# Performance work log

Measured on AMD Instinct MI355X. Metric: run time of the kernel, lower is better.

## Reference

```python
import jax, jax.numpy as jnp
import numpy as np

B, D, T, K = 32768, 1024, 100, 4  # batch, input_dim, num_trees, 2**(tree_depth-1)

def setup_inputs() -> dict:
    key = jax.random.key(0)
    k1, k2, k3, k4, k5 = jax.random.split(key, 5)
    s1 = 1.0 / np.sqrt(D)
    s2 = 1.0 / np.sqrt(K)
    return {
        "x": jax.random.normal(k1, (B, D), dtype=jnp.float32),
        "W1": jax.random.uniform(k2, (T, K, D), jnp.float32, -s1, s1),  # per-tree first Linear
        "b1": jax.random.uniform(k3, (T, K), jnp.float32, -s1, s1),
        "final_weight": jnp.full((T,), 1.0 / T, dtype=jnp.float32),
        "fc_w": jax.random.uniform(k4, (2, K), jnp.float32, -s2, s2),
        "fc_b": jax.random.uniform(k5, (2,), jnp.float32, -s2, s2),
    }

def reference(x, W1, b1, final_weight, fc_w, fc_b):
    # split_probs for all trees at once: [B, T, K]
    split = jnp.einsum("bd,tkd->btk", x, W1) + b1[None, :, :]
    leaf = jax.nn.sigmoid(split)  # tree[1] is Sigmoid applied to split_probs
    # sum(split.unsqueeze(1)*leaf.unsqueeze(2), -1) == leaf * sum_k(split)
    tree_out = leaf * jnp.sum(split, axis=-1, keepdims=True)  # [B, T, K]
    weighted = jnp.einsum("btk,t->bk", tree_out, final_weight)  # [B, K]
    logits = weighted @ fc_w.T + fc_b  # [B, 2]
    return logits
```

## Files before the change

kernel.cpp:

```cpp
#include <hip/hip_runtime.h>
#include <hip/hip_bf16.h>


typedef __bf16 bf16x8 __attribute__((ext_vector_type(8)));
typedef float f32x4 __attribute__((ext_vector_type(4)));

#define B_ROWS 32768
#define D_DIM  1024
#define N_COLS 400
#define BM     128
#define BK     64
#define NCHUNK 16
#define THREADS 640
#define NTPW 5
#define MT   4

__device__ __forceinline__ unsigned short f2bf(float f) {
    unsigned int u = __float_as_uint(f);
    u += 0x7FFFu + ((u >> 16) & 1u);
    return (unsigned short)(u >> 16);
}
__device__ __forceinline__ unsigned int pk2(float a, float b) {
    return (unsigned int)f2bf(a) | ((unsigned int)f2bf(b) << 16);
}
__device__ __forceinline__ uint4 cvt8u(float4 a, float4 b) {
    uint4 u;
    u.x = pk2(a.x, a.y); u.y = pk2(a.z, a.w);
    u.z = pk2(b.x, b.y); u.w = pk2(b.z, b.w);
    return u;
}
__device__ __forceinline__ bf16x8 cvt8(float4 a, float4 b) {
    return __builtin_bit_cast(bf16x8, cvt8u(a, b));
}

__global__ void cvt_f32_bf16_kernel(const float* __restrict__ in,
                                    unsigned short* __restrict__ out) {
    size_t i = ((size_t)blockIdx.x * 256 + threadIdx.x) * 8;
    float4 v0 = *reinterpret_cast<const float4*>(in + i);
    float4 v1 = *reinterpret_cast<const float4*>(in + i + 4);
    *reinterpret_cast<uint4*>(out + i) = cvt8u(v0, v1);
}

__device__ __forceinline__ void gl_lds16(const unsigned short* g,
                                         unsigned short* l) {
    __builtin_amdgcn_global_load_lds(
        (const __attribute__((address_space(1))) unsigned int*)g,
        (__attribute__((address_space(3))) unsigned int*)l,
        16, 0, 0);
}

#define FOR_N_(OP, m) OP(m,0) OP(m,1) OP(m,2) OP(m,3) OP(m,4)
#define FOR_MN(OP) FOR_N_(OP,0) FOR_N_(OP,1) FOR_N_(OP,2) FOR_N_(OP,3)

#define DECL_ACC(m,n) f32x4 acc##m##n = {};
#define MFMA_MN(m,n) acc##m##n = __builtin_amdgcn_mfma_f32_16x16x32_bf16( \
        afr##m, bfr##n, acc##m##n, 0, 0, 0);

template <int MODE>
__global__ __launch_bounds__(THREADS, 1) void xgb_v8(
    const float* __restrict__ x,
    const void*  __restrict__ b_any,
    const float* __restrict__ b1,
    const float* __restrict__ fw,
    const float* __restrict__ fcw,
    const float* __restrict__ fcb,
    float* __restrict__ out)
{
    __shared__ __align__(16) unsigned short Abuf[2][BM * BK];
    __shared__ __align__(16) unsigned short Bbuf[2][N_COLS * BK];
    __shared__ float Pbuf[BM * NTPW * 2];

    const int tid  = threadIdx.x;
    const int wave = tid >> 6;
    const int lane = tid & 63;
    const int quad = lane >> 4;
    const int l15  = lane & 15;
    const int mh   = wave / 5;
    const int nf   = wave % 5;
    const int row0 = blockIdx.x * BM;

    FOR_MN(DECL_ACC)

    if (MODE == 0) {
        const unsigned short* w1b = (const unsigned short*)b_any;

#define BDECL(t) const unsigned short* bsrc##t; int bdst##t; \
        { const int s_ = wave + 10 * (t); const int rr_ = lane >> 3; \
          const int cc_ = ((lane & 7) - rr_) & 7; \
          bsrc##t = w1b + (size_t)(s_ * 8 + rr_) * D_DIM + cc_ * 8; \
          bdst##t = s_ * 512; }
        BDECL(0) BDECL(1) BDECL(2) BDECL(3) BDECL(4)

        const int r0a = tid >> 3,          c0a = tid & 7;
        const int r1a = (tid + 640) >> 3,  c1a = (tid + 640) & 7;
        const bool hasU1 = (tid < 384);
        const float* asrc0 = x + (size_t)(row0 + r0a) * D_DIM + c0a * 8;
        const float* asrc1 = x + (size_t)(row0 + r1a) * D_DIM + c1a * 8;
        const int adst0 = r0a * 64 + ((c0a + r0a) & 7) * 8;
        const int adst1 = r1a * 64 + ((c1a + r1a) & 7) * 8;
        float4 areg00, areg01, areg10, areg11;

#define LOADA(kc) do { \
        areg00 = *reinterpret_cast<const float4*>(asrc0 + (kc));     \
        areg01 = *reinterpret_cast<const float4*>(asrc0 + (kc) + 4); \
        if (hasU1) { \
            areg10 = *reinterpret_cast<const float4*>(asrc1 + (kc));     \
            areg11 = *reinterpret_cast<const float4*>(asrc1 + (kc) + 4); \
        } } while (0)

#define WRITEA(Ab) do { \
        *reinterpret_cast<uint4*>((Ab) + adst0) = cvt8u(areg00, areg01); \
        if (hasU1) \
            *reinterpret_cast<uint4*>((Ab) + adst1) = cvt8u(areg10, areg11); \
        } while (0)

#define STAGEB(kc, Bb) do { \
        gl_lds16(bsrc0 + (kc), (Bb) + bdst0); \
        gl_lds16(bsrc1 + (kc), (Bb) + bdst1); \
        gl_lds16(bsrc2 + (kc), (Bb) + bdst2); \
        gl_lds16(bsrc3 + (kc), (Bb) + bdst3); \
        gl_lds16(bsrc4 + (kc), (Bb) + bdst4); } while (0)

#define LOAD_AFR(m) { const int row_ = mh * 64 + (m) * 16 + l15; \
        const int p_ = (quad + h * 4 + row_) & 7; \
        afr##m = *reinterpret_cast<const bf16x8*>(Ab_ + row_ * 64 + p_ * 8); }
#define LOAD_BFR(n) { const int row_ = (nf * NTPW + (n)) * 16 + l15; \
        const int p_ = (quad + h * 4 + row_) & 7; \
        bfr##n = *reinterpret_cast<const bf16x8*>(Bb_ + row_ * 64 + p_ * 8); }

        LOADA(0);
        STAGEB(0, Bbuf[0]);
        WRITEA(Abuf[0]);

        #pragma unroll 1
        for (int c = 0; c < NCHUNK; ++c) {
            const int cur = c & 1;
            const unsigned short* Ab_ = Abuf[cur];
            const unsigned short* Bb_ = Bbuf[cur];
            __syncthreads();
            if (c + 1 < NCHUNK) {
                LOADA((c + 1) * BK);
                STAGEB((c + 1) * BK, Bbuf[1 - cur]);
            }
            #pragma unroll
            for (int h = 0; h < 2; ++h) {
                bf16x8 afr0, afr1, afr2, afr3;
                bf16x8 bfr0, bfr1, bfr2, bfr3, bfr4;
                LOAD_AFR(0) LOAD_AFR(1) LOAD_AFR(2) LOAD_AFR(3)
                LOAD_BFR(0) LOAD_BFR(1) LOAD_BFR(2) LOAD_BFR(3) LOAD_BFR(4)
                FOR_MN(MFMA_MN)
            }
            if (c + 1 < NCHUNK) WRITEA(Abuf[1 - cur]);
        }
    } else {
        const float* af = x + (size_t)(row0 + mh * 64 + l15) * D_DIM + quad * 8;
        const float* bf32 = (const float*)b_any
                          + (size_t)((nf * NTPW) * 16 + l15) * D_DIM + quad * 8;
        for (int step = 0; step < 32; ++step) {
            const int off = step * 32;
            bf16x8 afr0, afr1, afr2, afr3;
            bf16x8 bfr0, bfr1, bfr2, bfr3, bfr4;
#define LOAD_AFR2(m) { \
            float4 a0_ = *reinterpret_cast<const float4*>(af + (size_t)(m) * 16 * D_DIM + off); \
            float4 a1_ = *reinterpret_cast<const float4*>(af + (size_t)(m) * 16 * D_DIM + off + 4); \
            afr##m = cvt8(a0_, a1_); }
#define LOAD_BFR2(n) { \
            float4 b0_ = *reinterpret_cast<const float4*>(bf32 + (size_t)(n) * 16 * D_DIM + off); \
            float4 b1_ = *reinterpret_cast<const float4*>(bf32 + (size_t)(n) * 16 * D_DIM + off + 4); \
            bfr##n = cvt8(b0_, b1_); }
            LOAD_AFR2(0) LOAD_AFR2(1) LOAD_AFR2(2) LOAD_AFR2(3)
            LOAD_BFR2(0) LOAD_BFR2(1) LOAD_BFR2(2) LOAD_BFR2(3) LOAD_BFR2(4)
            FOR_MN(MFMA_MN)
        }
    }

    const float fcw0 = fcw[l15 & 3];
    const float fcw1 = fcw[4 + (l15 & 3)];

#define PRE_N(n) \
    const float bias##n = b1[(nf * NTPW + (n)) * 16 + l15]; \
    const float tw##n   = fw[((nf * NTPW + (n)) * 16 + l15) >> 2];
    PRE_N(0) PRE_N(1) PRE_N(2) PRE_N(3) PRE_N(4)

#define EPI_TERM(m,r,n) { \
        const float split_ = acc##m##n[r] + bias##n; \
        float s_ = split_; \
        s_ += __shfl_xor(s_, 1); \
        s_ += __shfl_xor(s_, 2); \
        const float leaf_ = 1.0f / (1.0f + __expf(-split_)); \
        const float val_ = tw##n * leaf_ * s_; \
        q0 += val_ * fcw0; q1 += val_ * fcw1; }

#define EPI_ONE(m,r) { \
        float q0 = 0.f, q1 = 0.f; \
        EPI_TERM(m,r,0) EPI_TERM(m,r,1) EPI_TERM(m,r,2) \
        EPI_TERM(m,r,3) EPI_TERM(m,r,4) \
        q0 += __shfl_xor(q0, 1); q0 += __shfl_xor(q0, 2); \
        q0 += __shfl_xor(q0, 4); q0 += __shfl_xor(q0, 8); \
        q1 += __shfl_xor(q1, 1); q1 += __shfl_xor(q1, 2); \
        q1 += __shfl_xor(q1, 4); q1 += __shfl_xor(q1, 8); \
        const int row_ = mh * 64 + (m) * 16 + quad * 4 + (r); \
        if (l15 == 0) Pbuf[(row_ * NTPW + nf) * 2 + 0] = q0; \
        if (l15 == 1) Pbuf[(row_ * NTPW + nf) * 2 + 1] = q1; }

#define EPI_M(m) EPI_ONE(m,0) EPI_ONE(m,1) EPI_ONE(m,2) EPI_ONE(m,3)
    EPI_M(0) EPI_M(1) EPI_M(2) EPI_M(3)

    __syncthreads();

    if (tid < 2 * BM) {
        const int r = tid >> 1, j = tid & 1;
        float s = fcb[j];
        #pragma unroll
        for (int w = 0; w < NTPW; ++w)
            s += Pbuf[(r * NTPW + w) * 2 + j];
        out[(row0 + r) * 2 + j] = s;
    }
}

extern "C" void kernel_launch(void* const* d_in, const int* in_sizes, int n_in,
                              void* d_out, int out_size, void* d_ws, size_t ws_size,
                              hipStream_t stream) {
    const float* x   = (const float*)d_in[0];
    const float* W1  = (const float*)d_in[1];
    const float* b1  = (const float*)d_in[2];
    const float* fw  = (const float*)d_in[3];
    const float* fcw = (const float*)d_in[4];
    const float* fcb = (const float*)d_in[5];
    float* out = (float*)d_out;

    const size_t w1_elems = (size_t)N_COLS * D_DIM;
    if (ws_size >= w1_elems * sizeof(unsigned short)) {
        unsigned short* w1b = (unsigned short*)d_ws;
        cvt_f32_bf16_kernel<<<(int)(w1_elems / 2048), 256, 0, stream>>>(W1, w1b);
        xgb_v8<0><<<B_ROWS / BM, THREADS, 0, stream>>>(
            x, (const void*)w1b, b1, fw, fcw, fcb, out);
    } else {
        xgb_v8<2><<<B_ROWS / BM, THREADS, 0, stream>>>(
            x, (const void*)W1, b1, fw, fcw, fcb, out);
    }
}
```

Baseline: 235.5 us.

## Shrink block to 64 rows and 32-wide K chunks for multi-block occupancy

Halves the row tile and K chunk, cuts the block to five waves that each own one N-fragment group, and raises launch bounds to three blocks per CU. LDS swizzling is reworked for 32-wide rows. The goal is more resident blocks so they can hide global-load and sync latency. The cost is twice as many K iterations and barriers, and each W1 tile is now reused across fewer rows, so W1 traffic rises.

```diff
diff --git a/kernel.cpp b/kernel.cpp
--- a/kernel.cpp
+++ b/kernel.cpp
@@ -8,10 +8,10 @@
 #define B_ROWS 32768
 #define D_DIM  1024
 #define N_COLS 400
-#define BM     128
-#define BK     64
-#define NCHUNK 16
-#define THREADS 640
+#define BM     64
+#define BK     32
+#define NCHUNK 32
+#define THREADS 320
 #define NTPW 5
 #define MT   4
 
@@ -57,7 +57,7 @@
         afr##m, bfr##n, acc##m##n, 0, 0, 0);
 
 template <int MODE>
-__global__ __launch_bounds__(THREADS, 1) void xgb_v8(
+__global__ __launch_bounds__(THREADS, 3) void xgb_v9(
     const float* __restrict__ x,
     const void*  __restrict__ b_any,
     const float* __restrict__ b1,
@@ -75,8 +75,7 @@
     const int lane = tid & 63;
     const int quad = lane >> 4;
     const int l15  = lane & 15;
-    const int mh   = wave / 5;
-    const int nf   = wave % 5;
+    const int nf   = wave;
     const int row0 = blockIdx.x * BM;
 
     FOR_MN(DECL_ACC)
@@ -85,33 +84,25 @@
         const unsigned short* w1b = (const unsigned short*)b_any;
 
 #define BDECL(t) const unsigned short* bsrc##t; int bdst##t; \
-        { const int s_ = wave + 10 * (t); const int rr_ = lane >> 3; \
-          const int cc_ = ((lane & 7) - rr_) & 7; \
-          bsrc##t = w1b + (size_t)(s_ * 8 + rr_) * D_DIM + cc_ * 8; \
+        { const int s_ = wave + 5 * (t); const int rb_ = s_ * 16 + (lane >> 2); \
+          const int cc_ = ((lane & 3) - (rb_ >> 1)) & 3; \
+          bsrc##t = w1b + (size_t)rb_ * D_DIM + cc_ * 8; \
           bdst##t = s_ * 512; }
         BDECL(0) BDECL(1) BDECL(2) BDECL(3) BDECL(4)
 
-        const int r0a = tid >> 3,          c0a = tid & 7;
-        const int r1a = (tid + 640) >> 3,  c1a = (tid + 640) & 7;
-        const bool hasU1 = (tid < 384);
+        const int r0a = tid >> 2, c0a = tid & 3;
+        const bool doA = (tid < 256);
         const float* asrc0 = x + (size_t)(row0 + r0a) * D_DIM + c0a * 8;
-        const float* asrc1 = x + (size_t)(row0 + r1a) * D_DIM + c1a * 8;
-        const int adst0 = r0a * 64 + ((c0a + r0a) & 7) * 8;
-        const int adst1 = r1a * 64 + ((c1a + r1a) & 7) * 8;
-        float4 areg00, areg01, areg10, areg11;
-
-#define LOADA(kc) do { \
+        const int adst0 = r0a * 32 + ((c0a + (r0a >> 1)) & 3) * 8;
+        float4 areg00, areg01;
+
+#define LOADA(kc) do { if (doA) { \
         areg00 = *reinterpret_cast<const float4*>(asrc0 + (kc));     \
         areg01 = *reinterpret_cast<const float4*>(asrc0 + (kc) + 4); \
-        if (hasU1) { \
-            areg10 = *reinterpret_cast<const float4*>(asrc1 + (kc));     \
-            areg11 = *reinterpret_cast<const float4*>(asrc1 + (kc) + 4); \
         } } while (0)
 
-#define WRITEA(Ab) do { \
+#define WRITEA(Ab) do { if (doA) \
         *reinterpret_cast<uint4*>((Ab) + adst0) = cvt8u(areg00, areg01); \
-        if (hasU1) \
-            *reinterpret_cast<uint4*>((Ab) + adst1) = cvt8u(areg10, areg11); \
         } while (0)
 
 #define STAGEB(kc, Bb) do { \
@@ -121,12 +112,12 @@
         gl_lds16(bsrc3 + (kc), (Bb) + bdst3); \
         gl_lds16(bsrc4 + (kc), (Bb) + bdst4); } while (0)
 
-#define LOAD_AFR(m) { const int row_ = mh * 64 + (m) * 16 + l15; \
-        const int p_ = (quad + h * 4 + row_) & 7; \
-        afr##m = *reinterpret_cast<const bf16x8*>(Ab_ + row_ * 64 + p_ * 8); }
+#define LOAD_AFR(m) { const int row_ = (m) * 16 + l15; \
+        const int p_ = (quad + (row_ >> 1)) & 3; \
+        afr##m = *reinterpret_cast<const bf16x8*>(Ab_ + row_ * 32 + p_ * 8); }
 #define LOAD_BFR(n) { const int row_ = (nf * NTPW + (n)) * 16 + l15; \
-        const int p_ = (quad + h * 4 + row_) & 7; \
-        bfr##n = *reinterpret_cast<const bf16x8*>(Bb_ + row_ * 64 + p_ * 8); }
+        const int p_ = (quad + (row_ >> 1)) & 3; \
+        bfr##n = *reinterpret_cast<const bf16x8*>(Bb_ + row_ * 32 + p_ * 8); }
 
         LOADA(0);
         STAGEB(0, Bbuf[0]);
@@ -142,8 +133,7 @@
                 LOADA((c + 1) * BK);
                 STAGEB((c + 1) * BK, Bbuf[1 - cur]);
             }
-            #pragma unroll
-            for (int h = 0; h < 2; ++h) {
+            {
                 bf16x8 afr0, afr1, afr2, afr3;
                 bf16x8 bfr0, bfr1, bfr2, bfr3, bfr4;
                 LOAD_AFR(0) LOAD_AFR(1) LOAD_AFR(2) LOAD_AFR(3)
@@ -153,7 +143,7 @@
             if (c + 1 < NCHUNK) WRITEA(Abuf[1 - cur]);
         }
     } else {
-        const float* af = x + (size_t)(row0 + mh * 64 + l15) * D_DIM + quad * 8;
+        const float* af = x + (size_t)(row0 + l15) * D_DIM + quad * 8;
         const float* bf32 = (const float*)b_any
                           + (size_t)((nf * NTPW) * 16 + l15) * D_DIM + quad * 8;
         for (int step = 0; step < 32; ++step) {
@@ -199,7 +189,7 @@
         q0 += __shfl_xor(q0, 4); q0 += __shfl_xor(q0, 8); \
         q1 += __shfl_xor(q1, 1); q1 += __shfl_xor(q1, 2); \
         q1 += __shfl_xor(q1, 4); q1 += __shfl_xor(q1, 8); \
-        const int row_ = mh * 64 + (m) * 16 + quad * 4 + (r); \
+        const int row_ = (m) * 16 + quad * 4 + (r);            \
         if (l15 == 0) Pbuf[(row_ * NTPW + nf) * 2 + 0] = q0; \
         if (l15 == 1) Pbuf[(row_ * NTPW + nf) * 2 + 1] = q1; }
 
@@ -233,10 +223,10 @@
     if (ws_size >= w1_elems * sizeof(unsigned short)) {
         unsigned short* w1b = (unsigned short*)d_ws;
         cvt_f32_bf16_kernel<<<(int)(w1_elems / 2048), 256, 0, stream>>>(W1, w1b);
-        xgb_v8<0><<<B_ROWS / BM, THREADS, 0, stream>>>(
+        xgb_v9<0><<<B_ROWS / BM, THREADS, 0, stream>>>(
             x, (const void*)w1b, b1, fw, fcw, fcb, out);
     } else {
-        xgb_v8<2><<<B_ROWS / BM, THREADS, 0, stream>>>(
+        xgb_v9<2><<<B_ROWS / BM, THREADS, 0, stream>>>(
             x, (const void*)W1, b1, fw, fcw, fcb, out);
     }
 }
```

Measured after the change: 265.6 us. 12.8% more time.
